# Optimization experiments

Measured on AMD Instinct MI355X. Metric: run time of the kernel, lower is better.

## Reference

```python
import jax, jax.numpy as jnp
import numpy as np

B, S, HID = 2, 2048, 3072
H, KV, D = 16, 8, 256
EPS = 1e-6
SCALE = D ** -0.5  # query_pre_attn_scalar is None -> head_dim**-0.5
NEG = -1e9


def setup_inputs() -> dict:
    key = jax.random.key(0)
    ks = jax.random.split(key, 7)
    hidden_states = jax.random.normal(ks[0], (B, S, HID), jnp.float32)
    # rotary tables: freqs_cis = exp(i * pos * theta_j), theta_j = 10000^(-2j/D)
    pos = jnp.arange(S, dtype=jnp.float32)
    inv_freq = 1.0 / (10000.0 ** (jnp.arange(0, D, 2, dtype=jnp.float32) / D))  # [D/2]
    ang = pos[:, None] * inv_freq[None, :]  # [S, D/2]
    freqs_cos = jnp.cos(ang)
    freqs_sin = jnp.sin(ang)
    # additive causal mask [1,1,S,S]
    causal = jnp.tril(jnp.ones((S, S), dtype=bool))
    mask = jnp.where(causal, 0.0, NEG).astype(jnp.float32)[None, None]
    q_w = jax.random.normal(ks[1], (HID, H * D), jnp.float32) * 0.02
    k_w = jax.random.normal(ks[2], (HID, KV * D), jnp.float32) * 0.02
    v_w = jax.random.normal(ks[3], (HID, KV * D), jnp.float32) * 0.02
    o_w = jax.random.normal(ks[4], (H * D, HID), jnp.float32) * 0.02
    qnorm_w = jax.random.normal(ks[5], (D,), jnp.float32) * 0.1
    knorm_w = jax.random.normal(ks[6], (D,), jnp.float32) * 0.1
    return dict(hidden_states=hidden_states, freqs_cos=freqs_cos, freqs_sin=freqs_sin,
                mask=mask, q_w=q_w, k_w=k_w, v_w=v_w, o_w=o_w,
                qnorm_w=qnorm_w, knorm_w=knorm_w)


def rmsnorm(x, w, eps=EPS):
    # RMSNorm with add_unit_offset: x * rsqrt(mean(x^2)+eps) * (1 + w)
    x32 = x.astype(jnp.float32)
    n = x32 * jax.lax.rsqrt(jnp.mean(x32 * x32, axis=-1, keepdims=True) + eps)
    return (n * (1.0 + w.astype(jnp.float32))).astype(x.dtype)


def rope(x, cos, sin):
    # x: [B, S, Hx, D]; complex mult with (x1 + i x2), then concat(real, imag)
    x1, x2 = jnp.split(x, 2, axis=-1)  # each [B,S,Hx,D/2]
    c = cos[None, :, None, :]
    s = sin[None, :, None, :]
    return jnp.concatenate([x1 * c - x2 * s, x1 * s + x2 * c], axis=-1)


def reference(hidden_states, freqs_cos, freqs_sin, mask, q_w, k_w, v_w, o_w, qnorm_w, knorm_w):
    bsz, seqlen = hidden_states.shape[0], hidden_states.shape[1]
    xq = (hidden_states @ q_w).reshape(bsz, seqlen, H, D)
    xk = (hidden_states @ k_w).reshape(bsz, seqlen, KV, D)
    xv = (hidden_states @ v_w).reshape(bsz, seqlen, KV, D)
    # QK-norm (use_qk_norm=True)
    xq = rmsnorm(xq, qnorm_w)
    xk = rmsnorm(xk, knorm_w)
    # rotary embeddings
    xq = rope(xq, freqs_cos, freqs_sin)
    xk = rope(xk, freqs_cos, freqs_sin)
    # GQA: repeat kv heads to match query heads
    rep = H // KV
    xk = jnp.repeat(xk, rep, axis=2)
    xv = jnp.repeat(xv, rep, axis=2)
    q = jnp.transpose(xq, (0, 2, 1, 3)) * SCALE  # [B,H,S,D]
    k = jnp.transpose(xk, (0, 2, 1, 3))
    v = jnp.transpose(xv, (0, 2, 1, 3))
    scores = jnp.einsum('bhqd,bhkd->bhqk', q, k) + mask
    probs = jax.nn.softmax(scores.astype(jnp.float32), axis=-1).astype(q.dtype)
    out = jnp.einsum('bhqk,bhkd->bhqd', probs, v)
    out = jnp.transpose(out, (0, 2, 1, 3)).reshape(bsz, seqlen, H * D)
    return out @ o_w
```

## Files before the change

### kernel.cpp

```cpp
#include <hip/hip_runtime.h>
#include <hip/hip_bf16.h>
#include <cstdint>

#define B_   2
#define S_   2048
#define HID_ 3072
#define H_   16
#define KV_  8
#define D_   256
#define HD_  4096
#define KVD_ 2048
#define QKS_ 8192

constexpr float EPS_   = 1e-6f;
constexpr float SCALE_ = 0.0625f;

typedef unsigned short u16;
typedef __attribute__((ext_vector_type(8))) short bf16x8;
typedef __attribute__((ext_vector_type(4))) float f32x4;

__device__ inline float bf2f(u16 u) { return __uint_as_float(((unsigned int)u) << 16); }
__device__ inline u16 f2bf(float f) {
  unsigned int x = __float_as_uint(f);
  x += 0x7fffu + ((x >> 16) & 1u);
  return (u16)(x >> 16);
}

__device__ inline void gll16(const u16* g, u16* l) {
  __builtin_amdgcn_global_load_lds((const __attribute__((address_space(1))) unsigned int*)g,
                                   (__attribute__((address_space(3))) unsigned int*)l,
                                   16, 0, 0);
}

__global__ void cast_f32_bf16(const float* __restrict__ in, u16* __restrict__ out, int n4) {
  int i = blockIdx.x * blockDim.x + threadIdx.x;
  if (i < n4) {
    float4 v = ((const float4*)in)[i];
    ushort4 o;
    o.x = f2bf(v.x); o.y = f2bf(v.y); o.z = f2bf(v.z); o.w = f2bf(v.w);
    ((ushort4*)out)[i] = o;
  }
}

__global__ void transpose_cast(const float* __restrict__ in, u16* __restrict__ out, int K, int N) {
  __shared__ __align__(16) float tile[64][65];
  int n0 = blockIdx.x * 64, k0 = blockIdx.y * 64;
  int t = threadIdx.x;
  int rr = t >> 4, cc = (t & 15) * 4;
  for (int i = 0; i < 4; i++) {
    float4 v = *(const float4*)(&in[(size_t)(k0 + rr + 16 * i) * N + n0 + cc]);
    tile[rr + 16 * i][cc + 0] = v.x; tile[rr + 16 * i][cc + 1] = v.y;
    tile[rr + 16 * i][cc + 2] = v.z; tile[rr + 16 * i][cc + 3] = v.w;
  }
  __syncthreads();
  for (int i = 0; i < 4; i++) {
    int orow = rr + 16 * i;
    ushort4 o;
    o.x = f2bf(tile[cc + 0][orow]); o.y = f2bf(tile[cc + 1][orow]);
    o.z = f2bf(tile[cc + 2][orow]); o.w = f2bf(tile[cc + 3][orow]);
    *(ushort4*)(&out[(size_t)(n0 + orow) * K + k0 + cc]) = o;
  }
}

__global__ void transpose_v(const u16* __restrict__ in, u16* __restrict__ out) {
  __shared__ __align__(16) u16 tile[64][68];
  int n0 = blockIdx.x * 64, tk0 = blockIdx.y * 64;
  int b = tk0 >> 11, s0 = tk0 & (S_ - 1);
  int t = threadIdx.x;
  int rr = t >> 4, cc = (t & 15) * 4;
  for (int i = 0; i < 4; i++) {
    ushort4 v = *(const ushort4*)(&in[(size_t)(tk0 + rr + 16 * i) * QKS_ + n0 + cc]);
    tile[rr + 16 * i][cc + 0] = v.x; tile[rr + 16 * i][cc + 1] = v.y;
    tile[rr + 16 * i][cc + 2] = v.z; tile[rr + 16 * i][cc + 3] = v.w;
  }
  __syncthreads();
  for (int i = 0; i < 4; i++) {
    int orow = rr + 16 * i;
    ushort4 o;
    o.x = tile[cc + 0][orow]; o.y = tile[cc + 1][orow];
    o.z = tile[cc + 2][orow]; o.w = tile[cc + 3][orow];
    *(ushort4*)(&out[((size_t)b << 22) + (size_t)(n0 + orow) * S_ + s0 + cc]) = o;
  }
}

template <bool OUTF32>
__global__ __launch_bounds__(512, 2) void gemm256(const u16* __restrict__ A,
                                                  const u16* __restrict__ Bt,
                                                  void* __restrict__ Cv, int M, int N, int K) {
  __shared__ __align__(16) u16 As[2][16384];
  __shared__ __align__(16) u16 Bs[2][16384];
  int t = threadIdx.x, lane = t & 63, wave = t >> 6;
  int quad = lane >> 4, l16 = lane & 15;
  int wm = wave >> 2, wn = wave & 3;

  int nwg = gridDim.x * gridDim.y;
  int bid = blockIdx.y * gridDim.x + blockIdx.x;
  int sbid = (bid & 7) * (nwg >> 3) + (bid >> 3);
  int bn = (sbid % gridDim.x) * 256;
  int bm = (sbid / gridDim.x) * 256;

  int srow = lane >> 2;
  int scol8 = ((lane & 3) ^ ((lane >> 3) & 3)) * 8;
  const u16* ap = A + (size_t)(bm + srow) * K + scol8;
  const u16* bp = Bt + (size_t)(bn + srow) * K + scol8;
  int nr = (wave & 1) + ((wave >> 1) << 2);

  auto stA = [&](int sr, int sc, int k0, int bufi) {
    gll16(ap + (size_t)(sr * 16) * K + k0 + sc * 32, &As[bufi][(sr * 2 + sc) * 512]);
  };
  auto stB = [&](int sr, int sc, int k0, int bufi) {
    gll16(bp + (size_t)(sr * 16) * K + k0 + sc * 32, &Bs[bufi][(sr * 2 + sc) * 512]);
  };

  int rsw = l16 * 32 + ((quad ^ ((l16 >> 1) & 3)) * 8);
  auto LDA = [&](int bufi, int i, int ks) {
    return *(const bf16x8*)(&As[bufi][((wm * 8 + i) * 2 + ks) * 512 + rsw]);
  };
  auto LDB = [&](int bufi, int j, int ks) {
    return *(const bf16x8*)(&Bs[bufi][((wn * 4 + j) * 2 + ks) * 512 + rsw]);
  };

  f32x4 acc[8][4] = {};
  int NT = K >> 6;

#pragma unroll
  for (int h = 0; h < 2; h++) {
    int k0 = h * 64;
    stA(wave, 0, k0, h); stA(wave, 1, k0, h);
    stA(wave + 8, 0, k0, h); stA(wave + 8, 1, k0, h);
    stB(nr, 0, k0, h); stB(nr, 1, k0, h);
    stB(nr + 2, 0, k0, h); stB(nr + 2, 1, k0, h);
  }
  asm volatile("s_waitcnt vmcnt(8)" ::: "memory");
  __builtin_amdgcn_s_barrier();
  asm volatile("" ::: "memory");

  bf16x8 A0[4][2], B01[2][2];
#pragma unroll
  for (int j = 0; j < 2; j++) { B01[j][0] = LDB(0, j, 0); B01[j][1] = LDB(0, j, 1); }
#pragma unroll
  for (int i = 0; i < 4; i++) { A0[i][0] = LDA(0, i, 0); A0[i][1] = LDA(0, i, 1); }

#pragma unroll 1
  for (int kt = 0; kt < NT; kt++) {
    int cur = kt & 1, nxt = cur ^ 1;
    int kp = (kt + 2) * 64;
    bool rd_next = (kt + 1) < NT;
    bool pre2 = (kt + 2) < NT;
    bf16x8 A1[4][2], B23[2][2];

#pragma unroll
    for (int i = 0; i < 4; i++) { A1[i][0] = LDA(cur, i + 4, 0); A1[i][1] = LDA(cur, i + 4, 1); }
    asm volatile("s_waitcnt lgkmcnt(8)" ::: "memory");
    __builtin_amdgcn_s_setprio(1);
#pragma unroll
    for (int i = 0; i < 4; i++)
#pragma unroll
      for (int j = 0; j < 2; j++) {
        acc[i][j] = __builtin_amdgcn_mfma_f32_16x16x32_bf16(A0[i][0], B01[j][0], acc[i][j], 0, 0, 0);
        acc[i][j] = __builtin_amdgcn_mfma_f32_16x16x32_bf16(A0[i][1], B01[j][1], acc[i][j], 0, 0, 0);
      }
    __builtin_amdgcn_s_setprio(0);
    __builtin_amdgcn_s_barrier();
    asm volatile("" ::: "memory");

#pragma unroll
    for (int j = 0; j < 2; j++) { B23[j][0] = LDB(cur, j + 2, 0); B23[j][1] = LDB(cur, j + 2, 1); }
    if (pre2) { stA(wave, 0, kp, cur); stA(wave, 1, kp, cur); stB(nr, 0, kp, cur); }
    asm volatile("s_waitcnt lgkmcnt(4)" ::: "memory");
    __builtin_amdgcn_s_setprio(1);
#pragma unroll
    for (int i = 0; i < 4; i++)
#pragma unroll
      for (int j = 0; j < 2; j++) {
        acc[i + 4][j] = __builtin_amdgcn_mfma_f32_16x16x32_bf16(A1[i][0], B01[j][0], acc[i + 4][j], 0, 0, 0);
        acc[i + 4][j] = __builtin_amdgcn_mfma_f32_16x16x32_bf16(A1[i][1], B01[j][1], acc[i + 4][j], 0, 0, 0);
      }
    __builtin_amdgcn_s_setprio(0);
    if (pre2) asm volatile("s_waitcnt vmcnt(3)" ::: "memory");
    else      asm volatile("s_waitcnt vmcnt(0)" ::: "memory");
    __builtin_amdgcn_s_barrier();
    asm volatile("" ::: "memory");

    if (rd_next) {
#pragma unroll
      for (int j = 0; j < 2; j++) { B01[j][0] = LDB(nxt, j, 0); B01[j][1] = LDB(nxt, j, 1); }
    }
    if (pre2) { stB(nr, 1, kp, cur); stA(wave + 8, 0, kp, cur); stA(wave + 8, 1, kp, cur); }
    if (rd_next) asm volatile("s_waitcnt lgkmcnt(4)" ::: "memory");
    else         asm volatile("s_waitcnt lgkmcnt(0)" ::: "memory");
    __builtin_amdgcn_s_setprio(1);
#pragma unroll
    for (int i = 0; i < 4; i++)
#pragma unroll
      for (int j = 0; j < 2; j++) {
        acc[i][j + 2] = __builtin_amdgcn_mfma_f32_16x16x32_bf16(A0[i][0], B23[j][0], acc[i][j + 2], 0, 0, 0);
        acc[i][j + 2] = __builtin_amdgcn_mfma_f32_16x16x32_bf16(A0[i][1], B23[j][1], acc[i][j + 2], 0, 0, 0);
      }
    __builtin_amdgcn_s_setprio(0);
    __builtin_amdgcn_s_barrier();
    asm volatile("" ::: "memory");

    if (rd_next) {
#pragma unroll
      for (int i = 0; i < 4; i++) { A0[i][0] = LDA(nxt, i, 0); A0[i][1] = LDA(nxt, i, 1); }
    }
    if (pre2) { stB(nr + 2, 0, kp, cur); stB(nr + 2, 1, kp, cur); }
    __builtin_amdgcn_s_setprio(1);
#pragma unroll
    for (int i = 0; i < 4; i++)
#pragma unroll
      for (int j = 0; j < 2; j++) {
        acc[i + 4][j + 2] = __builtin_amdgcn_mfma_f32_16x16x32_bf16(A1[i][0], B23[j][0], acc[i + 4][j + 2], 0, 0, 0);
        acc[i + 4][j + 2] = __builtin_amdgcn_mfma_f32_16x16x32_bf16(A1[i][1], B23[j][1], acc[i + 4][j + 2], 0, 0, 0);
      }
    __builtin_amdgcn_s_setprio(0);
  }

#pragma unroll
  for (int i = 0; i < 8; i++)
#pragma unroll
    for (int j = 0; j < 4; j++)
#pragma unroll
      for (int r = 0; r < 4; r++) {
        int row = bm + wm * 128 + i * 16 + quad * 4 + r;
        int col = bn + wn * 64 + j * 16 + l16;
        float v = acc[i][j][r];
        if (OUTF32) ((float*)Cv)[(size_t)row * N + col] = v;
        else ((u16*)Cv)[(size_t)row * N + col] = f2bf(v);
      }
}

__global__ void rmsnorm_rope(u16* __restrict__ x, const float* __restrict__ w,
                             const float* __restrict__ fc, const float* __restrict__ fsn,
                             int nh, int stride, float outscale) {
  int token = blockIdx.x;
  int head = blockIdx.y * 4 + (threadIdx.x >> 6);
  if (head >= nh) return;
  int lane = threadIdx.x & 63;
  int s = token & (S_ - 1);
  u16* p = x + (size_t)token * stride + head * D_;
  float v0 = bf2f(p[lane]);
  float v1 = bf2f(p[lane + 64]);
  float v2 = bf2f(p[lane + 128]);
  float v3 = bf2f(p[lane + 192]);
  float ss = v0 * v0 + v1 * v1 + v2 * v2 + v3 * v3;
  for (int off = 32; off; off >>= 1) ss += __shfl_xor(ss, off, 64);
  float rs = rsqrtf(ss * (1.0f / D_) + EPS_);
  float n0 = v0 * rs * (1.0f + w[lane]);
  float n1 = v1 * rs * (1.0f + w[lane + 64]);
  float n2 = v2 * rs * (1.0f + w[lane + 128]);
  float n3 = v3 * rs * (1.0f + w[lane + 192]);
  float c0 = fc[s * 128 + lane], s0 = fsn[s * 128 + lane];
  float c1 = fc[s * 128 + lane + 64], s1 = fsn[s * 128 + lane + 64];
  p[lane]       = f2bf((n0 * c0 - n2 * s0) * outscale);
  p[lane + 128] = f2bf((n0 * s0 + n2 * c0) * outscale);
  p[lane + 64]  = f2bf((n1 * c1 - n3 * s1) * outscale);
  p[lane + 192] = f2bf((n1 * s1 + n3 * c1) * outscale);
}

__global__ __launch_bounds__(256, 3) void flash_attn(const u16* __restrict__ Q,
                                                     const u16* __restrict__ Kb,
                                                     const u16* __restrict__ Vt,
                                                     u16* __restrict__ O) {
  __shared__ __align__(16) u16 Ks[2][8 * 1024];
  __shared__ __align__(16) u16 Vs[8 * 1024];
  int t = threadIdx.x, lane = t & 63, wave = t >> 6;
  int quad = lane >> 4, l16 = lane & 15;
  int h = blockIdx.y, b = blockIdx.z;
  int kvh = h >> 1;

  int swz = ((lane & 3) ^ ((lane >> 2) & 3)) * 8;
  int rswz = (quad ^ (l16 & 3)) * 8;
  const u16* kst = Kb + (size_t)(b * S_ + (lane >> 2)) * QKS_ + kvh * D_ + wave * 64 + swz;
  const u16* vst = Vt + ((size_t)b << 22) + (size_t)(kvh * D_ + wave * 64 + (lane >> 2)) * S_ + swz;

  auto stageK = [&](int kt, int bufi) {
    u16* kdst = &Ks[bufi][wave * 2048];
    const u16* ksrc = kst + (size_t)(kt * 32) * QKS_;
#pragma unroll
    for (int c2 = 0; c2 < 2; c2++)
#pragma unroll
      for (int r = 0; r < 2; r++)
        gll16(ksrc + (size_t)(r * 16) * QKS_ + c2 * 32, kdst + c2 * 1024 + r * 512);
  };
  auto stageV = [&](int kt) {
    u16* vdst = &Vs[wave * 2048];
#pragma unroll
    for (int c = 0; c < 4; c++)
      gll16(vst + (size_t)(c * 16) * S_ + kt * 32, vdst + c * 512);
  };

#pragma unroll 1
  for (int half = 0; half < 2; half++) {
    int qb = (half == 0) ? (31 - (int)blockIdx.x) * 64 : (int)blockIdx.x * 64;
    int qw = qb + wave * 16;

    bf16x8 qf[8];
    const u16* qp = Q + ((size_t)(b * S_) + qw + l16) * QKS_ + h * D_;
#pragma unroll
    for (int c = 0; c < 8; c++) qf[c] = *(const bf16x8*)(qp + c * 32 + quad * 8);

    f32x4 o_acc[16] = {};
    float m_s = -3e38f, l_s = 0.f;

    int nkt = (qb + 64) >> 5;
    stageK(0, 0);
    stageV(0);
#pragma unroll 1
    for (int kt = 0; kt < nkt; kt++) {
      int cur = kt & 1;
      asm volatile("s_waitcnt vmcnt(4)" ::: "memory");
      __builtin_amdgcn_s_barrier();
      asm volatile("" ::: "memory");
      if (kt + 1 < nkt) stageK(kt + 1, cur ^ 1);

      f32x4 sc0 = {}, sc1 = {};
#pragma unroll
      for (int c = 0; c < 8; c++) {
        bf16x8 k0 = *(const bf16x8*)(&Ks[cur][c * 1024 + l16 * 32 + rswz]);
        bf16x8 k1 = *(const bf16x8*)(&Ks[cur][c * 1024 + (l16 + 16) * 32 + rswz]);
        sc0 = __builtin_amdgcn_mfma_f32_16x16x32_bf16(k0, qf[c], sc0, 0, 0, 0);
        sc1 = __builtin_amdgcn_mfma_f32_16x16x32_bf16(k1, qf[c], sc1, 0, 0, 0);
      }

      int qg = qw + l16;
      int kbase = kt * 32 + quad * 4;
      float p0[4], p1[4];
      float mx = -1e30f;
#pragma unroll
      for (int r = 0; r < 4; r++) {
        p0[r] = (kbase + r <= qg) ? sc0[r] : -1e30f;
        p1[r] = (kbase + 16 + r <= qg) ? sc1[r] : -1e30f;
        mx = fmaxf(mx, fmaxf(p0[r], p1[r]));
      }
      mx = fmaxf(mx, __shfl_xor(mx, 16));
      mx = fmaxf(mx, __shfl_xor(mx, 32));
      float mn = fmaxf(m_s, mx);
      bool chg = mn > m_s;
      float rsum = 0.f;
#pragma unroll
      for (int r = 0; r < 4; r++) {
        p0[r] = __expf(p0[r] - mn);
        p1[r] = __expf(p1[r] - mn);
        rsum += p0[r] + p1[r];
      }
      if (__any((int)chg)) {
        float alpha = __expf(m_s - mn);
        float ar[4];
#pragma unroll
        for (int r = 0; r < 4; r++) ar[r] = __shfl(alpha, quad * 20 + r);
#pragma unroll
        for (int nt = 0; nt < 16; nt++)
#pragma unroll
          for (int r = 0; r < 4; r++) o_acc[nt][r] *= ar[r];
        l_s *= alpha;
      }
      m_s = mn;
      rsum += __shfl_xor(rsum, 16);
      rsum += __shfl_xor(rsum, 32);
      l_s += rsum;

      unsigned int w_[4], x_[4], gl[4], gh[4], sn[4], rc[4];
      w_[0] = (unsigned)f2bf(p0[0]) | ((unsigned)f2bf(p0[1]) << 16);
      w_[1] = (unsigned)f2bf(p0[2]) | ((unsigned)f2bf(p0[3]) << 16);
      w_[2] = (unsigned)f2bf(p1[0]) | ((unsigned)f2bf(p1[1]) << 16);
      w_[3] = (unsigned)f2bf(p1[2]) | ((unsigned)f2bf(p1[3]) << 16);
#pragma unroll
      for (int i = 0; i < 4; i++) x_[i] = (unsigned)__shfl_xor((int)w_[i], 16);
      bool odd = (quad & 1) != 0;
      gl[0] = odd ? x_[0] : w_[0]; gl[1] = odd ? x_[1] : w_[1];
      gl[2] = odd ? w_[0] : x_[0]; gl[3] = odd ? w_[1] : x_[1];
      gh[0] = odd ? x_[2] : w_[2]; gh[1] = odd ? x_[3] : w_[3];
      gh[2] = odd ? w_[2] : x_[2]; gh[3] = odd ? w_[3] : x_[3];
#pragma unroll
      for (int i = 0; i < 4; i++) sn[i] = odd ? gl[i] : gh[i];
#pragma unroll
      for (int i = 0; i < 4; i++) rc[i] = (unsigned)__shfl_xor((int)sn[i], 32);
      union { unsigned int u[4]; bf16x8 v; } pfc;
#pragma unroll
      for (int i = 0; i < 4; i++)
        pfc.u[i] = (quad == 0) ? gl[i] : (quad == 3) ? gh[i] : rc[i];
      bf16x8 pf = pfc.v;

      if (kt + 1 < nkt) asm volatile("s_waitcnt vmcnt(4)" ::: "memory");
      else              asm volatile("s_waitcnt vmcnt(0)" ::: "memory");
      __builtin_amdgcn_s_barrier();
      asm volatile("" ::: "memory");

#pragma unroll
      for (int nt = 0; nt < 16; nt++) {
        bf16x8 vf = *(const bf16x8*)(&Vs[(nt * 16 + l16) * 32 + rswz]);
        o_acc[nt] = __builtin_amdgcn_mfma_f32_16x16x32_bf16(pf, vf, o_acc[nt], 0, 0, 0);
      }

      asm volatile("s_waitcnt lgkmcnt(0)" ::: "memory");
      __builtin_amdgcn_s_barrier();
      asm volatile("" ::: "memory");
      if (kt + 1 < nkt) stageV(kt + 1);
    }

    float invl = 1.0f / l_s;
    float inv_r[4];
#pragma unroll
    for (int r = 0; r < 4; r++) inv_r[r] = __shfl(invl, quad * 20 + r);
    for (int r = 0; r < 4; r++) {
      int qg2 = qw + quad * 4 + r;
      u16* op = O + ((size_t)(b * S_) + qg2) * HD_ + h * D_;
      for (int nt = 0; nt < 16; nt++) op[nt * 16 + l16] = f2bf(o_acc[nt][r] * inv_r[r]);
    }
  }
}

extern "C" void kernel_launch(void* const* d_in, const int* in_sizes, int n_in,
                              void* d_out, int out_size, void* d_ws, size_t ws_size,
                              hipStream_t stream) {
  const float* hs  = (const float*)d_in[0];
  const float* fc  = (const float*)d_in[1];
  const float* fsn = (const float*)d_in[2];
  const float* qw  = (const float*)d_in[4];
  const float* kw  = (const float*)d_in[5];
  const float* vw  = (const float*)d_in[6];
  const float* ow  = (const float*)d_in[7];
  const float* qnw = (const float*)d_in[8];
  const float* knw = (const float*)d_in[9];

  char* ws = (char*)d_ws;
  u16* x_bf   = (u16*)(ws + 0);
  u16* vt     = (u16*)(ws + 0);
  u16* wqkv_t = (u16*)(ws + 25165824);
  u16* kw_t   = (u16*)(ws + 50331648);
  u16* vw_t   = (u16*)(ws + 62914560);
  u16* ow_t   = (u16*)(ws + 75497472);
  u16* xqkv   = (u16*)(ws + 100663296);
  u16* attn   = (u16*)(ws + 25165824);

  cast_f32_bf16<<<12288, 256, 0, stream>>>(hs, x_bf, 4096 * 3072 / 4);
  transpose_cast<<<dim3(64, 48), 256, 0, stream>>>(qw, wqkv_t, 3072, 4096);
  transpose_cast<<<dim3(32, 48), 256, 0, stream>>>(kw, kw_t, 3072, 2048);
  transpose_cast<<<dim3(32, 48), 256, 0, stream>>>(vw, vw_t, 3072, 2048);
  transpose_cast<<<dim3(48, 64), 256, 0, stream>>>(ow, ow_t, 4096, 3072);

  gemm256<false><<<dim3(32, 16), 512, 0, stream>>>(x_bf, wqkv_t, xqkv, 4096, 8192, 3072);

  rmsnorm_rope<<<dim3(4096, 4), 256, 0, stream>>>(xqkv, qnw, fc, fsn, 16, QKS_, SCALE_);
  rmsnorm_rope<<<dim3(4096, 2), 256, 0, stream>>>(xqkv + 4096, knw, fc, fsn, 8, QKS_, 1.0f);

  transpose_v<<<dim3(32, 64), 256, 0, stream>>>(xqkv + 6144, vt);

  flash_attn<<<dim3(16, 16, 2), 256, 0, stream>>>(xqkv, xqkv + 4096, vt, attn);

  gemm256<true><<<dim3(12, 16), 512, 0, stream>>>(attn, ow_t, (float*)d_out, 4096, 3072, 4096);
}
```

Measured before the change: 758.1 us.

## Simplify GEMM main loop to one barrier per k-tile with bulk prefetch

Restructures the double-buffered GEMM main loop. The four barriers and the interleaved partial global-to-LDS prefetches per k-tile become a single full vmcnt/lgkmcnt drain and one barrier, followed by a whole-tile prefetch of tile kt+2. Most setprio toggles are dropped, and the next-tile fragment loads move to after the final MFMA groups. This cuts barrier and synchronisation overhead, but it serialises memory latency at the full vmcnt(0) wait and loses the fine-grained overlap of global loads with MFMA work.

```diff
diff --git a/kernel.cpp b/kernel.cpp
--- a/kernel.cpp
+++ b/kernel.cpp
@@ -111,6 +111,13 @@
   auto stB = [&](int sr, int sc, int k0, int bufi) {
     gll16(bp + (size_t)(sr * 16) * K + k0 + sc * 32, &Bs[bufi][(sr * 2 + sc) * 512]);
   };
+  auto stageTile = [&](int kt, int bufi) {
+    int k0 = kt * 64;
+    stA(wave, 0, k0, bufi); stA(wave, 1, k0, bufi);
+    stA(wave + 8, 0, k0, bufi); stA(wave + 8, 1, k0, bufi);
+    stB(nr, 0, k0, bufi); stB(nr, 1, k0, bufi);
+    stB(nr + 2, 0, k0, bufi); stB(nr + 2, 1, k0, bufi);
+  };
 
   int rsw = l16 * 32 + ((quad ^ ((l16 >> 1) & 3)) * 8);
   auto LDA = [&](int bufi, int i, int ks) {
@@ -123,19 +130,13 @@
   f32x4 acc[8][4] = {};
   int NT = K >> 6;
 
-#pragma unroll
-  for (int h = 0; h < 2; h++) {
-    int k0 = h * 64;
-    stA(wave, 0, k0, h); stA(wave, 1, k0, h);
-    stA(wave + 8, 0, k0, h); stA(wave + 8, 1, k0, h);
-    stB(nr, 0, k0, h); stB(nr, 1, k0, h);
-    stB(nr + 2, 0, k0, h); stB(nr + 2, 1, k0, h);
-  }
+  stageTile(0, 0);
+  stageTile(1, 1);
   asm volatile("s_waitcnt vmcnt(8)" ::: "memory");
   __builtin_amdgcn_s_barrier();
   asm volatile("" ::: "memory");
 
-  bf16x8 A0[4][2], B01[2][2];
+  bf16x8 A0[4][2], A1[4][2], B01[2][2], B23[2][2];
 #pragma unroll
   for (int j = 0; j < 2; j++) { B01[j][0] = LDB(0, j, 0); B01[j][1] = LDB(0, j, 1); }
 #pragma unroll
@@ -144,15 +145,10 @@
 #pragma unroll 1
   for (int kt = 0; kt < NT; kt++) {
     int cur = kt & 1, nxt = cur ^ 1;
-    int kp = (kt + 2) * 64;
-    bool rd_next = (kt + 1) < NT;
-    bool pre2 = (kt + 2) < NT;
-    bf16x8 A1[4][2], B23[2][2];
 
 #pragma unroll
     for (int i = 0; i < 4; i++) { A1[i][0] = LDA(cur, i + 4, 0); A1[i][1] = LDA(cur, i + 4, 1); }
     asm volatile("s_waitcnt lgkmcnt(8)" ::: "memory");
-    __builtin_amdgcn_s_setprio(1);
 #pragma unroll
     for (int i = 0; i < 4; i++)
 #pragma unroll
@@ -160,15 +156,9 @@
         acc[i][j] = __builtin_amdgcn_mfma_f32_16x16x32_bf16(A0[i][0], B01[j][0], acc[i][j], 0, 0, 0);
         acc[i][j] = __builtin_amdgcn_mfma_f32_16x16x32_bf16(A0[i][1], B01[j][1], acc[i][j], 0, 0, 0);
       }
-    __builtin_amdgcn_s_setprio(0);
-    __builtin_amdgcn_s_barrier();
-    asm volatile("" ::: "memory");
-
 #pragma unroll
     for (int j = 0; j < 2; j++) { B23[j][0] = LDB(cur, j + 2, 0); B23[j][1] = LDB(cur, j + 2, 1); }
-    if (pre2) { stA(wave, 0, kp, cur); stA(wave, 1, kp, cur); stB(nr, 0, kp, cur); }
     asm volatile("s_waitcnt lgkmcnt(4)" ::: "memory");
-    __builtin_amdgcn_s_setprio(1);
 #pragma unroll
     for (int i = 0; i < 4; i++)
 #pragma unroll
@@ -176,19 +166,11 @@
         acc[i + 4][j] = __builtin_amdgcn_mfma_f32_16x16x32_bf16(A1[i][0], B01[j][0], acc[i + 4][j], 0, 0, 0);
         acc[i + 4][j] = __builtin_amdgcn_mfma_f32_16x16x32_bf16(A1[i][1], B01[j][1], acc[i + 4][j], 0, 0, 0);
       }
-    __builtin_amdgcn_s_setprio(0);
-    if (pre2) asm volatile("s_waitcnt vmcnt(3)" ::: "memory");
-    else      asm volatile("s_waitcnt vmcnt(0)" ::: "memory");
+    asm volatile("s_waitcnt lgkmcnt(0)" ::: "memory");
+    asm volatile("s_waitcnt vmcnt(0)" ::: "memory");
     __builtin_amdgcn_s_barrier();
     asm volatile("" ::: "memory");
-
-    if (rd_next) {
-#pragma unroll
-      for (int j = 0; j < 2; j++) { B01[j][0] = LDB(nxt, j, 0); B01[j][1] = LDB(nxt, j, 1); }
-    }
-    if (pre2) { stB(nr, 1, kp, cur); stA(wave + 8, 0, kp, cur); stA(wave + 8, 1, kp, cur); }
-    if (rd_next) asm volatile("s_waitcnt lgkmcnt(4)" ::: "memory");
-    else         asm volatile("s_waitcnt lgkmcnt(0)" ::: "memory");
+    if (kt + 2 < NT) stageTile(kt + 2, cur);
     __builtin_amdgcn_s_setprio(1);
 #pragma unroll
     for (int i = 0; i < 4; i++)
@@ -198,14 +180,10 @@
         acc[i][j + 2] = __builtin_amdgcn_mfma_f32_16x16x32_bf16(A0[i][1], B23[j][1], acc[i][j + 2], 0, 0, 0);
       }
     __builtin_amdgcn_s_setprio(0);
-    __builtin_amdgcn_s_barrier();
-    asm volatile("" ::: "memory");
-
-    if (rd_next) {
-#pragma unroll
-      for (int i = 0; i < 4; i++) { A0[i][0] = LDA(nxt, i, 0); A0[i][1] = LDA(nxt, i, 1); }
+    if (kt + 1 < NT) {
+#pragma unroll
+      for (int j = 0; j < 2; j++) { B01[j][0] = LDB(nxt, j, 0); B01[j][1] = LDB(nxt, j, 1); }
     }
-    if (pre2) { stB(nr + 2, 0, kp, cur); stB(nr + 2, 1, kp, cur); }
     __builtin_amdgcn_s_setprio(1);
 #pragma unroll
     for (int i = 0; i < 4; i++)
@@ -215,6 +193,10 @@
         acc[i + 4][j + 2] = __builtin_amdgcn_mfma_f32_16x16x32_bf16(A1[i][1], B23[j][1], acc[i + 4][j + 2], 0, 0, 0);
       }
     __builtin_amdgcn_s_setprio(0);
+    if (kt + 1 < NT) {
+#pragma unroll
+      for (int i = 0; i < 4; i++) { A0[i][0] = LDA(nxt, i, 0); A0[i][1] = LDA(nxt, i, 1); }
+    }
   }
 
 #pragma unroll
```

Result: no change. 747.1 us (-1.5%).
